# Performance work log

Hardware: AMD Instinct MI355X
Metric: run time of the kernel (lower is better)

## Reference

```python
import jax, jax.numpy as jnp
import numpy as np

# --- static anchor geometry (exactly mirrors RPN._make_anchor_box) ---

def _valid_idx():
    scales = [64.0, 128.0, 256.0]
    ratios = [0.5, 1.0, 2.0]
    # (h, w) per anchor, normalized by 448
    anc = np.array([[s / np.sqrt(r), s * np.sqrt(r)] for s in scales for r in ratios]) / 448.0
    c = (np.arange(28) + 0.5) / 28.0
    cy = np.repeat(c, 28).reshape(28, 28)  # y varies along rows
    cx = np.tile(c, (28, 1))               # x varies along cols
    boxes = np.zeros((28, 28, 36))
    for a in range(9):
        boxes[..., 4 * a + 0] = cy
        boxes[..., 4 * a + 1] = cx
        boxes[..., 4 * a + 2] = anc[a, 0]
        boxes[..., 4 * a + 3] = anc[a, 1]
    b = boxes.reshape(-1, 4)  # [7056, 4] in yxhw
    y1 = b[:, 0] - b[:, 2] / 2
    x1 = b[:, 1] - b[:, 3] / 2
    y2 = b[:, 0] + b[:, 2] / 2
    x2 = b[:, 1] + b[:, 3] / 2
    return np.where((y1 > 0) & (x1 > 0) & (y2 < 28) & (x2 < 28))[0]

_VALID = _valid_idx()  # 4850 static indices

ROI_CLS_THRESHOLD = 0.9


def setup_inputs() -> dict:
    key = jax.random.key(0)
    ks = jax.random.split(key, 4)
    C = 2048
    return {
        'x': jax.random.normal(ks[0], (1, C, 28, 28), jnp.float32),
        'conv_w': jax.random.normal(ks[1], (C, C, 3, 3), jnp.float32) * 0.02,
        'conv_b': jnp.zeros((C,), jnp.float32),
        'reg_w': jax.random.normal(ks[2], (36, C), jnp.float32) * 0.02,
        'reg_b': jnp.zeros((36,), jnp.float32),
        'cls_w': jax.random.normal(ks[3], (9, C), jnp.float32) * 0.02,
        'cls_b': jnp.zeros((9,), jnp.float32),
    }


def reference(x, conv_w, conv_b, reg_w, reg_b, cls_w, cls_b):
    # Conv block: 3x3 conv + BatchNorm(identity at init: gamma=1, beta=0, running stats 0/1) + ReLU
    h = jax.lax.conv_general_dilated(
        x, conv_w, window_strides=(1, 1), padding=((1, 1), (1, 1)),
        dimension_numbers=('NCHW', 'OIHW', 'NCHW'))
    h = jax.nn.relu(h + conv_b[None, :, None, None])
    # 1x1 conv heads + sigmoid
    reg = jax.nn.sigmoid(jnp.einsum('bchw,oc->bohw', h, reg_w) + reg_b[None, :, None, None])  # [1,36,28,28]
    cls = jax.nn.sigmoid(jnp.einsum('bchw,oc->bohw', h, cls_w) + cls_b[None, :, None, None])  # [1,9,28,28]
    # exact replication of view/permute/squeeze + static valid-anchor gather
    reg = reg.reshape(1, 4, -1).transpose(0, 2, 1)[0][_VALID]  # [4850, 4]
    cls = cls.reshape(-1)[_VALID]                              # [4850]
    # inference path (gt=None): reg[cls > 0.9]; fixed-shape masked equivalent
    keep = cls > ROI_CLS_THRESHOLD
    return reg * keep[:, None]
```

## Files before the change

### kernel.cpp

```cpp
#include <hip/hip_runtime.h>
#include <cstdint>

typedef __attribute__((ext_vector_type(8))) short s8v;
typedef __attribute__((ext_vector_type(4))) float f4v;

__device__ __forceinline__ unsigned short bf16_rne(float f) {
    unsigned u = __float_as_uint(f);
    u += 0x7FFFu + ((u >> 16) & 1u);
    return (unsigned short)(u >> 16);
}
__device__ __forceinline__ float bf16f(unsigned short h) {
    return __uint_as_float(((unsigned)h) << 16);
}
__device__ __forceinline__ void cvt2(float a, float b, unsigned& hiw, unsigned& low) {
    unsigned ua = __float_as_uint(a), ub = __float_as_uint(b);
    unsigned ha = ua + 0x7FFFu + ((ua >> 16) & 1u);
    unsigned hb = ub + 0x7FFFu + ((ub >> 16) & 1u);
    hiw = (ha >> 16) | (hb & 0xFFFF0000u);
    float ra = a - __uint_as_float(ha & 0xFFFF0000u);
    float rb = b - __uint_as_float(hb & 0xFFFF0000u);
    unsigned la = __float_as_uint(ra), lb = __float_as_uint(rb);
    la += 0x7FFFu + ((la >> 16) & 1u);
    lb += 0x7FFFu + ((lb >> 16) & 1u);
    low = (la >> 16) | (lb & 0xFFFF0000u);
}
__device__ __forceinline__ void cvt2t(float a, float b, unsigned& hiw, unsigned& low) {
    unsigned ua = __float_as_uint(a), ub = __float_as_uint(b);
    hiw = (ua >> 16) | (ub & 0xFFFF0000u);
    float ra = a - __uint_as_float(ua & 0xFFFF0000u);
    float rb = b - __uint_as_float(ub & 0xFFFF0000u);
    unsigned la = __float_as_uint(ra), lb = __float_as_uint(rb);
    low = (la >> 16) | (lb & 0xFFFF0000u);
}
__device__ __forceinline__ void cvt8(float4 a, float4 b, s8v& hi, s8v& lo) {
    unsigned h0, h1, h2, h3, l0, l1, l2, l3;
    cvt2t(a.x, a.y, h0, l0);
    cvt2t(a.z, a.w, h1, l1);
    cvt2t(b.x, b.y, h2, l2);
    cvt2t(b.z, b.w, h3, l3);
    uint4 uh{h0, h1, h2, h3}, ul{l0, l1, l2, l3};
    hi = *(s8v*)&uh;
    lo = *(s8v*)&ul;
}

__global__ __launch_bounds__(256) void transpose_x(const float* __restrict__ x,
                                                   float* __restrict__ xt) {
    __shared__ float t[64][65];
    int c0 = blockIdx.x * 64, p0 = blockIdx.y * 64;
    int l = threadIdx.x & 63, g = threadIdx.x >> 6;
#pragma unroll
    for (int j = 0; j < 16; ++j) {
        int cc = j * 4 + g;
        int p = p0 + l;
        t[cc][l] = (p < 784) ? x[(size_t)(c0 + cc) * 784 + p] : 0.f;
    }
    __syncthreads();
#pragma unroll
    for (int j = 0; j < 16; ++j) {
        int pp = j * 4 + g;
        int p = p0 + pp;
        if (p < 784) xt[(size_t)p * 2048 + c0 + l] = t[l][pp];
    }
}

__global__ __launch_bounds__(256) void build_B(const float* __restrict__ xt,
                                               unsigned* __restrict__ Bhi,
                                               unsigned* __restrict__ Blo) {
    int p = blockIdx.x;
    int h = p / 28, w = p % 28;
#pragma unroll
    for (int it = 0; it < 4; ++it) {
        int cp = it * 256 + threadIdx.x;
        float va[18];
#pragma unroll
        for (int r = 0; r < 9; ++r) {
            int h2 = h + r / 3 - 1, w2 = w + r % 3 - 1;
            bool ok = (h2 >= 0) & (h2 < 28) & (w2 >= 0) & (w2 < 28);
            float2 v = ok ? ((const float2*)(xt + (size_t)(h2 * 28 + w2) * 2048))[cp]
                          : float2{0.f, 0.f};
            va[r] = v.x;
            va[9 + r] = v.y;
        }
        size_t base = (size_t)p * 9216 + (size_t)cp * 9;
#pragma unroll
        for (int d = 0; d < 9; ++d) {
            unsigned hw, lw;
            cvt2(va[2 * d], va[2 * d + 1], hw, lw);
            Bhi[base + d] = hw;
            Blo[base + d] = lw;
        }
    }
}

#define KCH 1152
#define NSTEP 36
#define LDS_BYTES 28672

__global__ __launch_bounds__(256, 4) void conv_gemm(const float* __restrict__ cw,
                                                    const char* __restrict__ wsb,
                                                    uint32_t offBhi, uint32_t offBlo,
                                                    float* __restrict__ part) {
    __shared__ char smem[LDS_BYTES];
    int tid = threadIdx.x;
    int lane = tid & 63, wave = tid >> 6;
    int bm0 = blockIdx.x * 128, bn0 = blockIdx.y * 112, z = blockIdx.z;

    uint32_t doff[4], dldsB[4];
#pragma unroll
    for (int j = 0; j < 4; ++j) {
        int i = j * 4 + wave;
        if (i >= 14) i -= 2;
        bool hiP = i < 7;
        int jj = hiP ? i : i - 7;
        int prow = jj * 16 + (lane >> 2);
        int pos = lane & 3;
        int gblk = pos ^ ((prow >> 1) & 3);
        uint32_t elem = (uint32_t)(bn0 + prow) * 18432 + (uint32_t)z * KCH + gblk * 8;
        doff[j] = (hiP ? offBhi : offBlo) + elem * 2;
        dldsB[j] = (hiP ? 0u : 7168u) + (uint32_t)jj * 1024;
    }

    int m = lane & 15, qd = lane >> 4;
    int sw = (m >> 1) & 3;
    uint32_t bpos = (uint32_t)m * 64 + (uint32_t)((qd ^ sw) * 16);

    const float4* ap0 = (const float4*)(cw + (size_t)(bm0 + wave * 32 + m) * 18432
                                        + (size_t)z * KCH + (size_t)qd * 8);
    const float4* ap1 = (const float4*)(cw + (size_t)(bm0 + wave * 32 + 16 + m) * 18432
                                        + (size_t)z * KCH + (size_t)qd * 8);

    f4v acc[2][7];
#pragma unroll
    for (int a = 0; a < 2; ++a)
#pragma unroll
        for (int b = 0; b < 7; ++b) acc[a][b] = f4v{0.f, 0.f, 0.f, 0.f};

#pragma unroll
    for (int j = 0; j < 4; ++j) {
        __builtin_amdgcn_global_load_lds(
            (const __attribute__((address_space(1))) void*)(wsb + doff[j]),
            (__attribute__((address_space(3))) void*)(smem + dldsB[j]), 16, 0, 0);
        doff[j] += 64;
    }
    s8v ah[2], al[2], ahn[2], aln[2];
    {
        float4 a0 = ap0[0], a1 = ap0[1], a2 = ap1[0], a3 = ap1[1];
        ap0 += 8;
        ap1 += 8;
        cvt8(a0, a1, ah[0], al[0]);
        cvt8(a2, a3, ah[1], al[1]);
    }
    __syncthreads();

#pragma unroll 2
    for (int step = 0; step < NSTEP; ++step) {
        char* smB = smem + (step & 1) * 14336;
        float4 a0, a1, a2, a3;
        if (step < NSTEP - 1) {
            char* smBn = smem + ((step & 1) ^ 1) * 14336;
#pragma unroll
            for (int j = 0; j < 4; ++j) {
                __builtin_amdgcn_global_load_lds(
                    (const __attribute__((address_space(1))) void*)(wsb + doff[j]),
                    (__attribute__((address_space(3))) void*)(smBn + dldsB[j]), 16, 0, 0);
                doff[j] += 64;
            }
            a0 = ap0[0];
            a1 = ap0[1];
            a2 = ap1[0];
            a3 = ap1[1];
            ap0 += 8;
            ap1 += 8;
        }

        __builtin_amdgcn_s_setprio(1);
#pragma unroll
        for (int nt = 0; nt < 7; ++nt) {
            s8v bh = *(const s8v*)(smB + bpos + nt * 1024);
            s8v bl = *(const s8v*)(smB + 7168 + bpos + nt * 1024);
#pragma unroll
            for (int mt = 0; mt < 2; ++mt) {
                acc[mt][nt] = __builtin_amdgcn_mfma_f32_16x16x32_bf16(ah[mt], bh, acc[mt][nt], 0, 0, 0);
                acc[mt][nt] = __builtin_amdgcn_mfma_f32_16x16x32_bf16(ah[mt], bl, acc[mt][nt], 0, 0, 0);
                acc[mt][nt] = __builtin_amdgcn_mfma_f32_16x16x32_bf16(al[mt], bh, acc[mt][nt], 0, 0, 0);
            }
        }
        __builtin_amdgcn_s_setprio(0);

        if (step < NSTEP - 1) {
            cvt8(a0, a1, ahn[0], aln[0]);
            cvt8(a2, a3, ahn[1], aln[1]);
        }
        __syncthreads();
        ah[0] = ahn[0];
        ah[1] = ahn[1];
        al[0] = aln[0];
        al[1] = aln[1];
    }

    float* pz = part + (size_t)z * 1605632;
#pragma unroll
    for (int mt = 0; mt < 2; ++mt) {
        int o = bm0 + wave * 32 + mt * 16 + qd * 4;
#pragma unroll
        for (int nt = 0; nt < 7; ++nt) {
            int p = bn0 + nt * 16 + m;
            *(float4*)(pz + (size_t)p * 2048 + o) =
                float4{acc[mt][nt].x, acc[mt][nt].y, acc[mt][nt].z, acc[mt][nt].w};
        }
    }
}

__constant__ int HMIN_d[9] = {3, 2, 1, 6, 4, 3, 11, 8, 6};
__constant__ int WMIN_d[9] = {1, 2, 3, 3, 4, 6, 6, 8, 11};

__global__ __launch_bounds__(256) void heads(const float* __restrict__ part,
                                             const float* __restrict__ conv_b,
                                             const float* __restrict__ reg_w,
                                             const float* __restrict__ reg_b,
                                             const float* __restrict__ cls_w,
                                             const float* __restrict__ cls_b,
                                             float* __restrict__ out) {
    int tid = threadIdx.x;
    int lane = tid & 63, wave = tid >> 6;
    int p = blockIdx.x;
    int ci = tid * 2;

    float4 h0 = ((const float4*)conv_b)[ci];
    float4 h1 = ((const float4*)conv_b)[ci + 1];
#pragma unroll
    for (int z = 0; z < 16; ++z) {
        const float4* pz = (const float4*)(part + (size_t)z * 1605632 + (size_t)p * 2048);
        float4 a = pz[ci], b = pz[ci + 1];
        h0.x += a.x; h0.y += a.y; h0.z += a.z; h0.w += a.w;
        h1.x += b.x; h1.y += b.y; h1.z += b.z; h1.w += b.w;
    }
    h0.x = fmaxf(h0.x, 0.f); h0.y = fmaxf(h0.y, 0.f);
    h0.z = fmaxf(h0.z, 0.f); h0.w = fmaxf(h0.w, 0.f);
    h1.x = fmaxf(h1.x, 0.f); h1.y = fmaxf(h1.y, 0.f);
    h1.z = fmaxf(h1.z, 0.f); h1.w = fmaxf(h1.w, 0.f);

    float s[45];
#pragma unroll
    for (int o = 0; o < 36; ++o) {
        float4 wa = ((const float4*)(reg_w + (size_t)o * 2048))[ci];
        float4 wb = ((const float4*)(reg_w + (size_t)o * 2048))[ci + 1];
        s[o] = h0.x * wa.x + h0.y * wa.y + h0.z * wa.z + h0.w * wa.w +
               h1.x * wb.x + h1.y * wb.y + h1.z * wb.z + h1.w * wb.w;
    }
#pragma unroll
    for (int a = 0; a < 9; ++a) {
        float4 wa = ((const float4*)(cls_w + (size_t)a * 2048))[ci];
        float4 wb = ((const float4*)(cls_w + (size_t)a * 2048))[ci + 1];
        s[36 + a] = h0.x * wa.x + h0.y * wa.y + h0.z * wa.z + h0.w * wa.w +
                    h1.x * wb.x + h1.y * wb.y + h1.z * wb.z + h1.w * wb.w;
    }

    __shared__ float wsum[4][45];
    __shared__ float fin[45];
#pragma unroll
    for (int o = 0; o < 45; ++o) {
        float v = s[o];
#pragma unroll
        for (int d = 1; d < 64; d <<= 1) v += __shfl_xor(v, d, 64);
        if (lane == 0) wsum[wave][o] = v;
    }
    __syncthreads();
    if (tid < 45) fin[tid] = wsum[0][tid] + wsum[1][tid] + wsum[2][tid] + wsum[3][tid];
    __syncthreads();

    if (tid < 9) {
        int ap = tid;
        int n = ap * 784 + p;
        int pix = n / 9, a2 = n % 9;
        int hh = pix / 28, ww = pix % 28;
        if (hh >= HMIN_d[a2] && ww >= WMIN_d[a2]) {
            int row = 0;
#pragma unroll
            for (int a3 = 0; a3 < 9; ++a3) {
                int hm = HMIN_d[a3], wm = WMIN_d[a3];
                int full = hh - hm; if (full < 0) full = 0;
                row += full * (28 - wm);
                if (hh >= hm) { int prt = ww - wm; if (prt < 0) prt = 0; row += prt; }
                if (a3 < a2 && hh >= hm && ww >= wm) row += 1;
            }
            float cl = fin[36 + ap] + cls_b[ap];
            float keep = (1.f / (1.f + expf(-cl)) > 0.9f) ? 1.f : 0.f;
#pragma unroll
            for (int q = 0; q < 4; ++q) {
                float rl = fin[q * 9 + ap] + reg_b[q * 9 + ap];
                out[row * 4 + q] = keep / (1.f + expf(-rl));
            }
        }
    }
}

extern "C" void kernel_launch(void* const* d_in, const int* in_sizes, int n_in,
                              void* d_out, int out_size, void* d_ws, size_t ws_size,
                              hipStream_t stream) {
    const float* x = (const float*)d_in[0];
    const float* conv_w = (const float*)d_in[1];
    const float* conv_b = (const float*)d_in[2];
    const float* reg_w = (const float*)d_in[3];
    const float* reg_b = (const float*)d_in[4];
    const float* cls_w = (const float*)d_in[5];
    const float* cls_b = (const float*)d_in[6];
    float* out = (float*)d_out;
    char* ws = (char*)d_ws;

    const size_t o_part = 0;
    const size_t o_xt = 0;
    const size_t o_Bhi = 102760448;
    const size_t o_Blo = 131661824;

    transpose_x<<<dim3(32, 13), 256, 0, stream>>>(x, (float*)(ws + o_xt));
    build_B<<<784, 256, 0, stream>>>((const float*)(ws + o_xt), (unsigned*)(ws + o_Bhi),
                                     (unsigned*)(ws + o_Blo));
    conv_gemm<<<dim3(16, 7, 16), 256, 0, stream>>>(conv_w, ws, (uint32_t)o_Bhi,
                                                   (uint32_t)o_Blo, (float*)(ws + o_part));
    heads<<<784, 256, 0, stream>>>((const float*)(ws + o_part), conv_b, reg_w, reg_b,
                                   cls_w, cls_b, out);
}
```

Measured before the change: 505.3 us.

## Single-buffer conv GEMM LDS, remap blocks to XCDs, stage build_B stores via LDS

The conv GEMM drops the double-buffered LDS B tile for a single 14 KB buffer. Each step now issues its global-to-LDS loads, syncs, then runs the MFMAs, and the setprio hints are removed. The block index is remapped so blocks on the same XCD share B column tiles and K chunks, aiming for better L2 reuse. build_B stages its converted hi/lo words in shared memory so the global stores are coalesced. The risk is that load latency is no longer overlapped with compute inside a block, and the design relies on higher occupancy to hide it.

```diff
diff --git a/kernel.cpp b/kernel.cpp
--- a/kernel.cpp
+++ b/kernel.cpp
@@ -4,14 +4,6 @@
 typedef __attribute__((ext_vector_type(8))) short s8v;
 typedef __attribute__((ext_vector_type(4))) float f4v;
 
-__device__ __forceinline__ unsigned short bf16_rne(float f) {
-    unsigned u = __float_as_uint(f);
-    u += 0x7FFFu + ((u >> 16) & 1u);
-    return (unsigned short)(u >> 16);
-}
-__device__ __forceinline__ float bf16f(unsigned short h) {
-    return __uint_as_float(((unsigned)h) << 16);
-}
 __device__ __forceinline__ void cvt2(float a, float b, unsigned& hiw, unsigned& low) {
     unsigned ua = __float_as_uint(a), ub = __float_as_uint(b);
     unsigned ha = ua + 0x7FFFu + ((ua >> 16) & 1u);
@@ -66,11 +58,12 @@
 __global__ __launch_bounds__(256) void build_B(const float* __restrict__ xt,
                                                unsigned* __restrict__ Bhi,
                                                unsigned* __restrict__ Blo) {
+    __shared__ unsigned sh[2304], sl[2304];
     int p = blockIdx.x;
     int h = p / 28, w = p % 28;
-#pragma unroll
+    int tid = threadIdx.x;
     for (int it = 0; it < 4; ++it) {
-        int cp = it * 256 + threadIdx.x;
+        int cp = it * 256 + tid;
         float va[18];
 #pragma unroll
         for (int r = 0; r < 9; ++r) {
@@ -81,20 +74,29 @@
             va[r] = v.x;
             va[9 + r] = v.y;
         }
-        size_t base = (size_t)p * 9216 + (size_t)cp * 9;
 #pragma unroll
         for (int d = 0; d < 9; ++d) {
             unsigned hw, lw;
             cvt2(va[2 * d], va[2 * d + 1], hw, lw);
-            Bhi[base + d] = hw;
-            Blo[base + d] = lw;
-        }
-    }
-}
-
+            sh[tid * 9 + d] = hw;
+            sl[tid * 9 + d] = lw;
+        }
+        __syncthreads();
+        size_t gbase = (size_t)p * 9216 + (size_t)it * 2304;
+#pragma unroll
+        for (int j = 0; j < 9; ++j) {
+            Bhi[gbase + j * 256 + tid] = sh[j * 256 + tid];
+            Blo[gbase + j * 256 + tid] = sl[j * 256 + tid];
+        }
+        __syncthreads();
+    }
+}
+
+#define BHI_OFF 0
+#define BLO_OFF 7168
+#define LDS_BYTES 14336
 #define KCH 1152
 #define NSTEP 36
-#define LDS_BYTES 28672
 
 __global__ __launch_bounds__(256, 4) void conv_gemm(const float* __restrict__ cw,
                                                     const char* __restrict__ wsb,
@@ -103,9 +105,16 @@
     __shared__ char smem[LDS_BYTES];
     int tid = threadIdx.x;
     int lane = tid & 63, wave = tid >> 6;
-    int bm0 = blockIdx.x * 128, bn0 = blockIdx.y * 112, z = blockIdx.z;
-
-    uint32_t doff[4], dldsB[4];
+
+    int lin = blockIdx.x + (blockIdx.y << 4) + blockIdx.z * 112;
+    int xcd = lin & 7;
+    int g = lin >> 3;
+    int pairg = xcd * 14 + (g >> 4);
+    int bm0 = (g & 15) * 128;
+    int bn0 = (pairg % 7) * 112;
+    int z = pairg / 7;
+
+    uint32_t doff[4], dlds[4];
 #pragma unroll
     for (int j = 0; j < 4; ++j) {
         int i = j * 4 + wave;
@@ -117,7 +126,7 @@
         int gblk = pos ^ ((prow >> 1) & 3);
         uint32_t elem = (uint32_t)(bn0 + prow) * 18432 + (uint32_t)z * KCH + gblk * 8;
         doff[j] = (hiP ? offBhi : offBlo) + elem * 2;
-        dldsB[j] = (hiP ? 0u : 7168u) + (uint32_t)jj * 1024;
+        dlds[j] = (hiP ? BHI_OFF : BLO_OFF) + jj * 1024;
     }
 
     int m = lane & 15, qd = lane >> 4;
@@ -135,14 +144,7 @@
 #pragma unroll
         for (int b = 0; b < 7; ++b) acc[a][b] = f4v{0.f, 0.f, 0.f, 0.f};
 
-#pragma unroll
-    for (int j = 0; j < 4; ++j) {
-        __builtin_amdgcn_global_load_lds(
-            (const __attribute__((address_space(1))) void*)(wsb + doff[j]),
-            (__attribute__((address_space(3))) void*)(smem + dldsB[j]), 16, 0, 0);
-        doff[j] += 64;
-    }
-    s8v ah[2], al[2], ahn[2], aln[2];
+    s8v ah[2], al[2];
     {
         float4 a0 = ap0[0], a1 = ap0[1], a2 = ap1[0], a3 = ap1[1];
         ap0 += 8;
@@ -150,21 +152,17 @@
         cvt8(a0, a1, ah[0], al[0]);
         cvt8(a2, a3, ah[1], al[1]);
     }
-    __syncthreads();
-
-#pragma unroll 2
+
     for (int step = 0; step < NSTEP; ++step) {
-        char* smB = smem + (step & 1) * 14336;
+#pragma unroll
+        for (int j = 0; j < 4; ++j) {
+            __builtin_amdgcn_global_load_lds(
+                (const __attribute__((address_space(1))) void*)(wsb + doff[j]),
+                (__attribute__((address_space(3))) void*)(smem + dlds[j]), 16, 0, 0);
+            doff[j] += 64;
+        }
         float4 a0, a1, a2, a3;
         if (step < NSTEP - 1) {
-            char* smBn = smem + ((step & 1) ^ 1) * 14336;
-#pragma unroll
-            for (int j = 0; j < 4; ++j) {
-                __builtin_amdgcn_global_load_lds(
-                    (const __attribute__((address_space(1))) void*)(wsb + doff[j]),
-                    (__attribute__((address_space(3))) void*)(smBn + dldsB[j]), 16, 0, 0);
-                doff[j] += 64;
-            }
             a0 = ap0[0];
             a1 = ap0[1];
             a2 = ap1[0];
@@ -172,12 +170,12 @@
             ap0 += 8;
             ap1 += 8;
         }
-
-        __builtin_amdgcn_s_setprio(1);
+        __syncthreads();
+
 #pragma unroll
         for (int nt = 0; nt < 7; ++nt) {
-            s8v bh = *(const s8v*)(smB + bpos + nt * 1024);
-            s8v bl = *(const s8v*)(smB + 7168 + bpos + nt * 1024);
+            s8v bh = *(const s8v*)(smem + BHI_OFF + bpos + nt * 1024);
+            s8v bl = *(const s8v*)(smem + BLO_OFF + bpos + nt * 1024);
 #pragma unroll
             for (int mt = 0; mt < 2; ++mt) {
                 acc[mt][nt] = __builtin_amdgcn_mfma_f32_16x16x32_bf16(ah[mt], bh, acc[mt][nt], 0, 0, 0);
@@ -185,17 +183,12 @@
                 acc[mt][nt] = __builtin_amdgcn_mfma_f32_16x16x32_bf16(al[mt], bh, acc[mt][nt], 0, 0, 0);
             }
         }
-        __builtin_amdgcn_s_setprio(0);
 
         if (step < NSTEP - 1) {
-            cvt8(a0, a1, ahn[0], aln[0]);
-            cvt8(a2, a3, ahn[1], aln[1]);
+            cvt8(a0, a1, ah[0], al[0]);
+            cvt8(a2, a3, ah[1], al[1]);
         }
         __syncthreads();
-        ah[0] = ahn[0];
-        ah[1] = ahn[1];
-        al[0] = aln[0];
-        al[1] = aln[1];
     }
 
     float* pz = part + (size_t)z * 1605632;
```

After: 515.5 us. 2.0% more time.
